# Optimization experiments

Hardware: AMD Instinct MI355X
Metric: run time of the kernel (lower is better)

## Reference

```python
import jax, jax.numpy as jnp
import numpy as np

D_MODEL = 256
N_HEADS = 8
D_K = 16
LN_EPS = 1e-5


def setup_inputs() -> dict:
    key = jax.random.key(0)
    ks = jax.random.split(key, 10)
    B, S = 4, 2048
    inp = {
        "input_Q": jax.random.normal(ks[0], (B, S, D_MODEL), dtype=jnp.float32),
        "input_K": jax.random.normal(ks[1], (B, S, D_MODEL), dtype=jnp.float32),
        "input_V": jax.random.normal(ks[2], (B, S, D_MODEL), dtype=jnp.float32),
        "attn_mask": jax.random.randint(ks[3], (B, S, S), 0, 2) == 1,
        # learned params (torch Linear weight [out,in] stored here as [in,out])
        "Wq": jax.random.normal(ks[4], (D_MODEL, N_HEADS * D_K), dtype=jnp.float32) * (1.0 / np.sqrt(D_MODEL)),
        "Wk": jax.random.normal(ks[5], (D_MODEL, N_HEADS * D_K), dtype=jnp.float32) * (1.0 / np.sqrt(D_MODEL)),
        "Wv": jax.random.normal(ks[6], (D_MODEL, N_HEADS * D_K), dtype=jnp.float32) * (1.0 / np.sqrt(D_MODEL)),
        "Wfc": jax.random.normal(ks[7], (N_HEADS * D_K, D_MODEL), dtype=jnp.float32) * (1.0 / np.sqrt(N_HEADS * D_K)),
        "ln_gamma": jnp.ones((D_MODEL,), dtype=jnp.float32),
        "ln_beta": jnp.zeros((D_MODEL,), dtype=jnp.float32),
    }
    return inp


def reference(input_Q, input_K, input_V, attn_mask, Wq, Wk, Wv, Wfc, ln_gamma, ln_beta):
    B, S, _ = input_Q.shape
    # projections -> [B, H, S, d_k]
    Q = (input_Q @ Wq).reshape(B, S, N_HEADS, D_K).transpose(0, 2, 1, 3)
    K = (input_K @ Wk).reshape(B, S, N_HEADS, D_K).transpose(0, 2, 1, 3)
    V = (input_V @ Wv).reshape(B, S, N_HEADS, D_K).transpose(0, 2, 1, 3)
    # scores [B, H, S, S], masked softmax
    scores = jnp.einsum("bhqd,bhkd->bhqk", Q, K) / np.sqrt(D_K).astype(np.float32)
    scores = jnp.where(attn_mask[:, None, :, :], jnp.float32(-1e9), scores)
    attn = jax.nn.softmax(scores, axis=-1)
    context = jnp.einsum("bhqk,bhkd->bhqd", attn, V)
    context = context.transpose(0, 2, 1, 3).reshape(B, S, N_HEADS * D_K)
    out = context @ Wfc
    # LayerNorm (no residual in the original module)
    mu = jnp.mean(out, axis=-1, keepdims=True)
    var = jnp.var(out, axis=-1, keepdims=True)
    out = (out - mu) * jax.lax.rsqrt(var + LN_EPS) * ln_gamma + ln_beta
    return out
```

## Files before the change

kernel.cpp:

```cpp
#include <hip/hip_runtime.h>
#include <hip/hip_bf16.h>

#define S_LEN 2048
#define BATCH 4
#define NH 8
#define DK 16
#define DM 256
#define DP 128
#define L2E 1.4426950408889634f

typedef short bf16x8 __attribute__((ext_vector_type(8)));
typedef short short4v __attribute__((ext_vector_type(4)));
typedef float f32x16 __attribute__((ext_vector_type(16)));

__device__ __forceinline__ short f2bf(float x) {
    __hip_bfloat16 h = __float2bfloat16(x);
    return __builtin_bit_cast(short, h);
}

union Frag { bf16x8 v; short4v h2[2]; };

__global__ __launch_bounds__(256) void main1(
    const void* __restrict__ mraw, unsigned long long* __restrict__ ms64,
    const float* __restrict__ Xq, const float* __restrict__ Xk, const float* __restrict__ Xv,
    const float* __restrict__ Wq, const float* __restrict__ Wk, const float* __restrict__ Wv,
    short* __restrict__ Qt, short* __restrict__ Kb, short* __restrict__ Vb)
{
    __shared__ short xs_s[32 * 260];
    __shared__ int isBool;
    const int bi = blockIdx.x;
    const int t = threadIdx.x;

    if (bi < 768) {
        const int inp = bi >> 8;
        const int s0 = (bi & 255) * 32;
        {
            const float* xbase = ((inp == 0) ? Xq : (inp == 1) ? Xk : Xv) + (size_t)s0 * 256;
            #pragma unroll
            for (int u = 0; u < 8; ++u) {
                const int idx = u * 1024 + t * 4;
                const int row = idx >> 8, col = idx & 255;
                float4 xv = *(const float4*)(xbase + idx);
                short4v o = { f2bf(xv.x), f2bf(xv.y), f2bf(xv.z), f2bf(xv.w) };
                *(short4v*)&xs_s[row * 260 + col] = o;
            }
        }

        const int wave = t >> 6, lane = t & 63;
        const int lq = lane & 31, hi = lane >> 5;
        const int c = wave * 32 + lq;

        const float* W = (inp == 0) ? Wq : (inp == 1) ? Wk : Wv;
        const float scale = (inp == 0) ? 0.25f * L2E : 1.0f;
        Frag wf[16];
        #pragma unroll
        for (int kb = 0; kb < 16; ++kb) {
            const int k0 = kb * 16 + 4 * hi;
            union { bf16x8 v; short s[8]; } o;
            #pragma unroll
            for (int e = 0; e < 4; ++e) {
                o.s[e]     = f2bf(W[(size_t)(k0 + e) * DP + c] * scale);
                o.s[4 + e] = f2bf(W[(size_t)(k0 + 8 + e) * DP + c] * scale);
            }
            wf[kb].v = o.v;
        }
        __syncthreads();

        f32x16 acc;
        #pragma unroll
        for (int i = 0; i < 16; ++i) acc[i] = 0.f;

        #pragma unroll
        for (int kb = 0; kb < 16; ++kb) {
            Frag af;
            af.h2[0] = *(const short4v*)&xs_s[lq * 260 + kb*16 + 4*hi];
            af.h2[1] = *(const short4v*)&xs_s[lq * 260 + kb*16 + 8 + 4*hi];
            acc = __builtin_amdgcn_mfma_f32_32x32x16_bf16(af.v, wf[kb].v, acc, 0, 0, 0);
        }

        const int b = s0 >> 11, sl = s0 & (S_LEN - 1);
        const int h = c >> 4, d = c & 15;
        if (inp == 1) {
            #pragma unroll
            for (int r = 0; r < 16; ++r) {
                const int s = sl + (r & 3) + 8*(r >> 2) + 4*hi;
                Kb[(((size_t)(b * NH + h)) * S_LEN + s) * DK + d] = f2bf(acc[r]);
            }
        } else {
            short* base = (inp == 0)
                ? Qt + (((size_t)(b * NH + h)) * 16 + d) * S_LEN + sl
                : Vb + (((size_t)(b * NH + h)) * 32 + d) * S_LEN + sl;
            #pragma unroll
            for (int g = 0; g < 4; ++g) {
                short4v vv = { f2bf(acc[4*g]), f2bf(acc[4*g+1]), f2bf(acc[4*g+2]), f2bf(acc[4*g+3]) };
                *(short4v*)(base + 8*g + 4*hi) = vv;
            }
        }
    } else if (bi < 1280) {
        const int tid = (bi - 768) * 256 + t;
        const int bh = tid >> 12;
        const int rem = tid & 4095;
        const int row = 16 + (rem >> 11) * 4;
        const int s = rem & 2047;
        Vb[((size_t)bh * 32 + row) * S_LEN + s] = (short)0x3F80;
    } else {
        const int lane = t & 63;
        const size_t kbase0 = (size_t)(bi - 1280) * 4096;
        const size_t kbase = kbase0 + (size_t)(t >> 6) * 1024;

        union { uint4 v; unsigned u[4]; } uu;
        uu.v = *(const uint4*)((const unsigned char*)mraw + kbase + 16 * lane);

        if (t == 0) isBool = 0;
        __syncthreads();
        if ((uu.u[0] | uu.u[1] | uu.u[2] | uu.u[3]) & 0xFFFFFF00u) isBool = 1;
        __syncthreads();

        unsigned val16;
        if (isBool) {
            unsigned n0 = ((uu.u[0] & 0x01010101u) * 0x01020408u) >> 24;
            unsigned n1 = ((uu.u[1] & 0x01010101u) * 0x01020408u) >> 24;
            unsigned n2 = ((uu.u[2] & 0x01010101u) * 0x01020408u) >> 24;
            unsigned n3 = ((uu.u[3] & 0x01010101u) * 0x01020408u) >> 24;
            val16 = n0 | (n1 << 4) | (n2 << 8) | (n3 << 12);
        } else {
            const int* p = (const int*)mraw + kbase + 16 * lane;
            val16 = 0;
            #pragma unroll
            for (int cc = 0; cc < 16; ++cc) val16 |= (p[cc] != 0 ? 1u : 0u) << cc;
        }

        const int src0 = (4 * lane) & 63;
        const unsigned a0 = (unsigned)__shfl((int)val16, src0);
        const unsigned a1 = (unsigned)__shfl((int)val16, src0 + 1);
        const unsigned a2 = (unsigned)__shfl((int)val16, src0 + 2);
        const unsigned a3 = (unsigned)__shfl((int)val16, src0 + 3);

        if (lane < 16) {
            const unsigned long long w64 =
                (unsigned long long)a0 | ((unsigned long long)a1 << 16) |
                ((unsigned long long)a2 << 32) | ((unsigned long long)a3 << 48);
            const size_t row = kbase >> 11;
            const int w0 = (int)(kbase & 2047) >> 6;
            ms64[row * 32 + w0 + lane] = w64;
        }
    }
}

__global__ __launch_bounds__(256, 8) void attn_mfma(
    const short* __restrict__ Qt, const short* __restrict__ Kb, const short* __restrict__ Vb,
    const unsigned long long* __restrict__ ms64, float* __restrict__ pacc, float* __restrict__ pl)
{
    __shared__ short kt_s[128 * 20];
    __shared__ short vt_s[32 * 132];

    const int bh = blockIdx.y;
    const int b = bh >> 3;
    const int z = blockIdx.z;
    const int t = threadIdx.x;
    const int wave = t >> 6, lane = t & 63;
    const int lq = lane & 31, hi = lane >> 5;
    const int qrow = blockIdx.x * 128 + wave * 32 + lq;

    Frag qf;
    {
        const short* qt = Qt + (size_t)bh * 16 * S_LEN + qrow;
        #pragma unroll
        for (int j = 0; j < 4; ++j) {
            qf.h2[0][j] = qt[(size_t)(4*hi + j) * S_LEN];
            qf.h2[1][j] = qt[(size_t)(8 + 4*hi + j) * S_LEN];
        }
    }

    f32x16 acc;
    #pragma unroll
    for (int i = 0; i < 16; ++i) acc[i] = 0.f;

    const short* kbase = Kb + (size_t)bh * S_LEN * DK;
    const short* vbase = Vb + (size_t)bh * 32 * S_LEN;
    const unsigned long long* mrow = ms64 + ((size_t)b * S_LEN + qrow) * 32;

    const int tiles = (S_LEN / 128) / gridDim.z;
    const int t0 = z * tiles, t1 = t0 + tiles;

    for (int tile = t0; tile < t1; ++tile) {
        const int k0 = tile * 128;

        {
            const uint4 kv = *(const uint4*)(kbase + (size_t)k0 * DK + t * 8);
            short* kdst = &kt_s[(t >> 1) * 20 + (t & 1) * 8];
            *(uint2*)(kdst)     = *(uint2*)&kv;
            *(uint2*)(kdst + 4) = *((uint2*)&kv + 1);

            const short* vsrc = vbase + (size_t)(t >> 3) * S_LEN + k0 + (t & 7) * 16;
            uint4 v0 = *(const uint4*)(vsrc);
            uint4 v1 = *(const uint4*)(vsrc + 8);
            short* vdst = &vt_s[(t >> 3) * 132 + (t & 7) * 16];
            *(uint2*)(vdst)      = *(uint2*)&v0;
            *(uint2*)(vdst + 4)  = *((uint2*)&v0 + 1);
            *(uint2*)(vdst + 8)  = *(uint2*)&v1;
            *(uint2*)(vdst + 12) = *((uint2*)&v1 + 1);
        }
        __syncthreads();

        const ulonglong2 mw = *(const ulonglong2*)(mrow + tile * 2);
        const unsigned long long W64a = mw.x, W64b = mw.y;

        #pragma unroll
        for (int kt = 0; kt < 4; ++kt) {
            const unsigned int W = (unsigned int)(((kt < 2) ? W64a : W64b)
                                                  >> (32*(kt & 1) + 4*hi));
            f32x16 ci;
            #pragma unroll
            for (int r = 0; r < 16; ++r) {
                const int bit = (r & 3) + 8*(r >> 2);
                ci[r] = __int_as_float(((int)(W << (31 - bit)) >> 31) & 0xC2C80000);
            }

            Frag kf;
            kf.h2[0] = *(const short4v*)&kt_s[(kt*32 + lq) * 20 + 4*hi];
            kf.h2[1] = *(const short4v*)&kt_s[(kt*32 + lq) * 20 + 8 + 4*hi];
            f32x16 p = __builtin_amdgcn_mfma_f32_32x32x16_bf16(kf.v, qf.v, ci, 0, 0, 0);

            #pragma unroll
            for (int r = 0; r < 16; ++r) p[r] = __builtin_amdgcn_exp2f(p[r]);

            #pragma unroll
            for (int j = 0; j < 2; ++j) {
                union { bf16x8 v; unsigned int u[4]; } pf;
                #pragma unroll
                for (int e = 0; e < 4; ++e) {
                    asm("v_cvt_pk_bf16_f32 %0, %1, %2"
                        : "=v"(pf.u[e]) : "v"(p[j*8 + 2*e]), "v"(p[j*8 + 2*e + 1]));
                }
                Frag vf;
                const int vo = lq * 132 + (kt*2 + j) * 16 + 4*hi;
                vf.h2[0] = *(const short4v*)&vt_s[vo];
                vf.h2[1] = *(const short4v*)&vt_s[vo + 8];
                acc = __builtin_amdgcn_mfma_f32_32x32x16_bf16(vf.v, pf.v, acc, 0, 0, 0);
            }
        }
        __syncthreads();
    }

    float* pb = pacc + (((size_t)z * (BATCH*NH) + bh) * S_LEN + qrow) * 16;
    float4 o1 = { acc[0], acc[1], acc[2], acc[3] };
    float4 o2 = { acc[4], acc[5], acc[6], acc[7] };
    *(float4*)(pb + 4*hi) = o1;
    *(float4*)(pb + 8 + 4*hi) = o2;
    if (hi == 0) pl[((size_t)z * (BATCH*NH) + bh) * S_LEN + qrow] = acc[8];
}

__global__ __launch_bounds__(256) void fc_ln(
    const float* __restrict__ pacc, const float* __restrict__ pl, int ns,
    const float* __restrict__ Wfc,
    const float* __restrict__ gamma, const float* __restrict__ beta,
    float* __restrict__ out)
{
    __shared__ float cs[8][DP];
    __shared__ float ys[8][256];
    __shared__ float red[16];
    const int t = threadIdx.x;
    const int row0 = blockIdx.x * 8;

    {
        const int idx = t * 4;
        const int r = idx >> 7, k = idx & 127;
        const int grow = row0 + r;
        const int b = grow >> 11, q = grow & (S_LEN - 1);
        const int h = k >> 4, d0 = k & 15;
        float4 s = {0.f, 0.f, 0.f, 0.f};
        float L = 0.f;
        for (int z = 0; z < ns; ++z) {
            const size_t o = ((size_t)z * (BATCH*NH) + b * NH + h) * S_LEN + q;
            const float4 a = *(const float4*)(pacc + o * 16 + d0);
            s.x += a.x; s.y += a.y; s.z += a.z; s.w += a.w;
            L += pl[o];
        }
        const float inv = 1.0f / L;
        float4 o4 = { s.x * inv, s.y * inv, s.z * inv, s.w * inv };
        *(float4*)&cs[r][k] = o4;
    }
    __syncthreads();

    float acc[8] = {0,0,0,0,0,0,0,0};
    for (int k = 0; k < DP; k += 4) {
        const float w0 = Wfc[(k+0)*DM + t];
        const float w1 = Wfc[(k+1)*DM + t];
        const float w2 = Wfc[(k+2)*DM + t];
        const float w3 = Wfc[(k+3)*DM + t];
        #pragma unroll
        for (int r = 0; r < 8; ++r) {
            float4 x = *(const float4*)&cs[r][k];
            acc[r] = fmaf(x.x, w0, fmaf(x.y, w1, fmaf(x.z, w2, fmaf(x.w, w3, acc[r]))));
        }
    }

    #pragma unroll
    for (int r = 0; r < 8; ++r) ys[r][t] = acc[r];
    __syncthreads();

    const int w = t >> 6, lj = t & 63;
    #pragma unroll
    for (int rr = 0; rr < 2; ++rr) {
        const int r = w * 2 + rr;
        float a0 = ys[r][lj], a1 = ys[r][lj+64], a2 = ys[r][lj+128], a3 = ys[r][lj+192];
        float s1 = a0 + a1 + a2 + a3;
        float s2 = a0*a0 + a1*a1 + a2*a2 + a3*a3;
        #pragma unroll
        for (int off = 32; off; off >>= 1) {
            s1 += __shfl_xor(s1, off);
            s2 += __shfl_xor(s2, off);
        }
        if (lj == 0) {
            float mu = s1 * (1.0f/256.0f);
            float var = s2 * (1.0f/256.0f) - mu*mu;
            red[r*2]     = mu;
            red[r*2 + 1] = rsqrtf(var + 1e-5f);
        }
    }
    __syncthreads();

    const float g = gamma[t], be = beta[t];
    #pragma unroll
    for (int r = 0; r < 8; ++r) {
        float y = (acc[r] - red[r*2]) * red[r*2 + 1];
        out[(size_t)(row0 + r) * DM + t] = fmaf(y, g, be);
    }
}

extern "C" void kernel_launch(void* const* d_in, const int* in_sizes, int n_in,
                              void* d_out, int out_size, void* d_ws, size_t ws_size,
                              hipStream_t stream)
{
    const float* Xq = (const float*)d_in[0];
    const float* Xk = (const float*)d_in[1];
    const float* Xv = (const float*)d_in[2];
    const void* mask_raw = d_in[3];
    const float* Wq  = (const float*)d_in[4];
    const float* Wk  = (const float*)d_in[5];
    const float* Wv  = (const float*)d_in[6];
    const float* Wfc = (const float*)d_in[7];
    const float* gamma = (const float*)d_in[8];
    const float* beta  = (const float*)d_in[9];
    float* out = (float*)d_out;

    const size_t headsz = (size_t)BATCH * NH * S_LEN * DK;
    const size_t maskelems = (size_t)BATCH * S_LEN * S_LEN;

    char* wsb = (char*)d_ws;
    short* Qt = (short*)wsb;
    short* Kb = Qt + headsz;
    short* Vb = Kb + headsz;
    unsigned long long* msk = (unsigned long long*)(Vb + 2 * headsz);
    float* pacc = (float*)(msk + maskelems / 64);
    size_t ns = 4;
    {
        const size_t fixed = (size_t)((char*)pacc - wsb);
        while (ns > 1 && fixed + ns * ((size_t)BATCH*NH*S_LEN*17*4) > ws_size)
            ns >>= 1;
    }
    float* pl = pacc + ns * (size_t)BATCH * NH * S_LEN * 16;

    main1<<<dim3(768 + 512 + (unsigned)(maskelems / 4096)), dim3(256), 0, stream>>>(
        mask_raw, msk, Xq, Xk, Xv, Wq, Wk, Wv, Qt, Kb, Vb);
    attn_mfma<<<dim3(S_LEN / 128, BATCH * NH, (unsigned)ns), dim3(256), 0, stream>>>(
        Qt, Kb, Vb, msk, pacc, pl);
    fc_ln<<<dim3(BATCH * S_LEN / 8), dim3(256), 0, stream>>>(pacc, pl, (int)ns, Wfc, gamma, beta, out);
}
```

Baseline: 71.32 us.

## Store split-K partial attention outputs in bf16 and process 16 rows per fc_ln block

The attention kernel now packs its unnormalized partial context accumulators to bf16 before writing them to the workspace, which halves the bytes written and re-read between attn_mfma and fc_ln. fc_ln unpacks the bf16 values and sums them in fp32. Each fc_ln block also handles 16 rows instead of 8, so every Wfc load is reused across twice as many rows. The costs are rounding error in the partial sums, which are stored before normalization, plus more registers and LDS per fc_ln block and half as many blocks.

```diff
diff --git a/kernel.cpp b/kernel.cpp
--- a/kernel.cpp
+++ b/kernel.cpp
@@ -16,6 +16,9 @@
 __device__ __forceinline__ short f2bf(float x) {
     __hip_bfloat16 h = __float2bfloat16(x);
     return __builtin_bit_cast(short, h);
+}
+__device__ __forceinline__ float bf2f(short x) {
+    return __int_as_float(((int)(unsigned short)x) << 16);
 }
 
 union Frag { bf16x8 v; short4v h2[2]; };
@@ -149,7 +152,7 @@
 
 __global__ __launch_bounds__(256, 8) void attn_mfma(
     const short* __restrict__ Qt, const short* __restrict__ Kb, const short* __restrict__ Vb,
-    const unsigned long long* __restrict__ ms64, float* __restrict__ pacc, float* __restrict__ pl)
+    const unsigned long long* __restrict__ ms64, short* __restrict__ paccb, float* __restrict__ pl)
 {
     __shared__ short kt_s[128 * 20];
     __shared__ short vt_s[32 * 132];
@@ -185,7 +188,6 @@
 
     for (int tile = t0; tile < t1; ++tile) {
         const int k0 = tile * 128;
-
         {
             const uint4 kv = *(const uint4*)(kbase + (size_t)k0 * DK + t * 8);
             short* kdst = &kt_s[(t >> 1) * 20 + (t & 1) * 8];
@@ -243,67 +245,77 @@
         __syncthreads();
     }
 
-    float* pb = pacc + (((size_t)z * (BATCH*NH) + bh) * S_LEN + qrow) * 16;
-    float4 o1 = { acc[0], acc[1], acc[2], acc[3] };
-    float4 o2 = { acc[4], acc[5], acc[6], acc[7] };
-    *(float4*)(pb + 4*hi) = o1;
-    *(float4*)(pb + 8 + 4*hi) = o2;
+    short* pb = paccb + (((size_t)z * (BATCH*NH) + bh) * S_LEN + qrow) * 16;
+    union { short4v h; unsigned u[2]; } o1, o2;
+    asm("v_cvt_pk_bf16_f32 %0, %1, %2" : "=v"(o1.u[0]) : "v"(acc[0]), "v"(acc[1]));
+    asm("v_cvt_pk_bf16_f32 %0, %1, %2" : "=v"(o1.u[1]) : "v"(acc[2]), "v"(acc[3]));
+    asm("v_cvt_pk_bf16_f32 %0, %1, %2" : "=v"(o2.u[0]) : "v"(acc[4]), "v"(acc[5]));
+    asm("v_cvt_pk_bf16_f32 %0, %1, %2" : "=v"(o2.u[1]) : "v"(acc[6]), "v"(acc[7]));
+    *(short4v*)(pb + 4*hi) = o1.h;
+    *(short4v*)(pb + 8 + 4*hi) = o2.h;
     if (hi == 0) pl[((size_t)z * (BATCH*NH) + bh) * S_LEN + qrow] = acc[8];
 }
 
 __global__ __launch_bounds__(256) void fc_ln(
-    const float* __restrict__ pacc, const float* __restrict__ pl, int ns,
+    const short* __restrict__ paccb, const float* __restrict__ pl, int ns,
     const float* __restrict__ Wfc,
     const float* __restrict__ gamma, const float* __restrict__ beta,
     float* __restrict__ out)
 {
-    __shared__ float cs[8][DP];
-    __shared__ float ys[8][256];
-    __shared__ float red[16];
+    __shared__ float cs[16][DP];
+    __shared__ float ys[16][256];
+    __shared__ float red[32];
     const int t = threadIdx.x;
-    const int row0 = blockIdx.x * 8;
+    const int row0 = blockIdx.x * 16;
 
     {
-        const int idx = t * 4;
+        const int idx = t * 8;
         const int r = idx >> 7, k = idx & 127;
         const int grow = row0 + r;
         const int b = grow >> 11, q = grow & (S_LEN - 1);
         const int h = k >> 4, d0 = k & 15;
-        float4 s = {0.f, 0.f, 0.f, 0.f};
+        float s[8] = {0,0,0,0,0,0,0,0};
         float L = 0.f;
         for (int z = 0; z < ns; ++z) {
             const size_t o = ((size_t)z * (BATCH*NH) + b * NH + h) * S_LEN + q;
-            const float4 a = *(const float4*)(pacc + o * 16 + d0);
-            s.x += a.x; s.y += a.y; s.z += a.z; s.w += a.w;
+            const short4v a0 = *(const short4v*)(paccb + o * 16 + d0);
+            const short4v a1 = *(const short4v*)(paccb + o * 16 + d0 + 4);
+            #pragma unroll
+            for (int i = 0; i < 4; ++i) {
+                s[i]     += bf2f(a0[i]);
+                s[4 + i] += bf2f(a1[i]);
+            }
             L += pl[o];
         }
         const float inv = 1.0f / L;
-        float4 o4 = { s.x * inv, s.y * inv, s.z * inv, s.w * inv };
-        *(float4*)&cs[r][k] = o4;
+        #pragma unroll
+        for (int i = 0; i < 8; ++i) cs[r][k + i] = s[i] * inv;
     }
     __syncthreads();
 
-    float acc[8] = {0,0,0,0,0,0,0,0};
+    float acc[16];
+    #pragma unroll
+    for (int r = 0; r < 16; ++r) acc[r] = 0.f;
     for (int k = 0; k < DP; k += 4) {
         const float w0 = Wfc[(k+0)*DM + t];
         const float w1 = Wfc[(k+1)*DM + t];
         const float w2 = Wfc[(k+2)*DM + t];
         const float w3 = Wfc[(k+3)*DM + t];
         #pragma unroll
-        for (int r = 0; r < 8; ++r) {
+        for (int r = 0; r < 16; ++r) {
             float4 x = *(const float4*)&cs[r][k];
             acc[r] = fmaf(x.x, w0, fmaf(x.y, w1, fmaf(x.z, w2, fmaf(x.w, w3, acc[r]))));
         }
     }
 
     #pragma unroll
-    for (int r = 0; r < 8; ++r) ys[r][t] = acc[r];
+    for (int r = 0; r < 16; ++r) ys[r][t] = acc[r];
     __syncthreads();
 
     const int w = t >> 6, lj = t & 63;
     #pragma unroll
-    for (int rr = 0; rr < 2; ++rr) {
-        const int r = w * 2 + rr;
+    for (int rr = 0; rr < 4; ++rr) {
+        const int r = w * 4 + rr;
         float a0 = ys[r][lj], a1 = ys[r][lj+64], a2 = ys[r][lj+128], a3 = ys[r][lj+192];
         float s1 = a0 + a1 + a2 + a3;
         float s2 = a0*a0 + a1*a1 + a2*a2 + a3*a3;
@@ -323,7 +335,7 @@
 
     const float g = gamma[t], be = beta[t];
     #pragma unroll
-    for (int r = 0; r < 8; ++r) {
+    for (int r = 0; r < 16; ++r) {
         float y = (acc[r] - red[r*2]) * red[r*2 + 1];
         out[(size_t)(row0 + r) * DM + t] = fmaf(y, g, be);
     }
@@ -353,18 +365,18 @@
     short* Kb = Qt + headsz;
     short* Vb = Kb + headsz;
     unsigned long long* msk = (unsigned long long*)(Vb + 2 * headsz);
-    float* pacc = (float*)(msk + maskelems / 64);
+    short* paccb = (short*)(msk + maskelems / 64);
     size_t ns = 4;
     {
-        const size_t fixed = (size_t)((char*)pacc - wsb);
-        while (ns > 1 && fixed + ns * ((size_t)BATCH*NH*S_LEN*17*4) > ws_size)
+        const size_t fixed = (size_t)((char*)paccb - wsb);
+        while (ns > 1 && fixed + ns * ((size_t)BATCH*NH*S_LEN*(16*2 + 4)) > ws_size)
             ns >>= 1;
     }
-    float* pl = pacc + ns * (size_t)BATCH * NH * S_LEN * 16;
+    float* pl = (float*)(paccb + ns * (size_t)BATCH * NH * S_LEN * 16);
 
     main1<<<dim3(768 + 512 + (unsigned)(maskelems / 4096)), dim3(256), 0, stream>>>(
         mask_raw, msk, Xq, Xk, Xv, Wq, Wk, Wv, Qt, Kb, Vb);
     attn_mfma<<<dim3(S_LEN / 128, BATCH * NH, (unsigned)ns), dim3(256), 0, stream>>>(
-        Qt, Kb, Vb, msk, pacc, pl);
-    fc_ln<<<dim3(BATCH * S_LEN / 8), dim3(256), 0, stream>>>(pacc, pl, (int)ns, Wfc, gamma, beta, out);
-}
+        Qt, Kb, Vb, msk, paccb, pl);
+    fc_ln<<<dim3(BATCH * S_LEN / 16), dim3(256), 0, stream>>>(paccb, pl, (int)ns, Wfc, gamma, beta, out);
+}
```

Result: no change. 70.94 us (-0.5%).
